# Kernel optimization log

Hardware: AMD Instinct MI355X
Metric: run time of the kernel (lower is better)

The kernel has to match this reference:

```python
import jax, jax.numpy as jnp
import numpy as np

WINDOW_SIZE = 11
SIGMA = 1.5
DATA_RANGE = 1.0
C1 = (0.01 * DATA_RANGE) ** 2
C2 = (0.03 * DATA_RANGE) ** 2


def _gaussian_window(size: int, sigma: float) -> jnp.ndarray:
    coords = jnp.arange(size, dtype=jnp.float32) - size // 2
    g = jnp.exp(-(coords ** 2) / (2.0 * sigma ** 2))
    g = g / g.sum()
    w2d = g[:, None] * g[None, :]
    return w2d[None, None, :, :]  # (O=1, I=1, K, K)


def _conv_same(x, window):
    pad = WINDOW_SIZE // 2
    return jax.lax.conv_general_dilated(
        x, window,
        window_strides=(1, 1),
        padding=((pad, pad), (pad, pad)),
        dimension_numbers=("NCHW", "OIHW", "NCHW"),
    )


def setup_inputs() -> dict:
    key = jax.random.key(0)
    kx, ky = jax.random.split(key)
    B, C, H, W = 64, 1, 512, 512
    x = jax.random.uniform(kx, (B, C, H, W), dtype=jnp.float32)
    y = jax.random.uniform(ky, (B, C, H, W), dtype=jnp.float32)
    return {"x": x, "y": y}


def reference(x, y):
    window = _gaussian_window(WINDOW_SIZE, SIGMA)
    mu_x = _conv_same(x, window)
    mu_y = _conv_same(y, window)
    mu_x_sq = mu_x * mu_x
    mu_y_sq = mu_y * mu_y
    mu_xy = mu_x * mu_y
    sigma_x_sq = _conv_same(x * x, window) - mu_x_sq
    sigma_y_sq = _conv_same(y * y, window) - mu_y_sq
    sigma_xy = _conv_same(x * y, window) - mu_xy
    num = (2.0 * mu_xy + C1) * (2.0 * sigma_xy + C2)
    den = (mu_x_sq + mu_y_sq + C1) * (sigma_x_sq + sigma_y_sq + C2)
    ssim_map = num / den
    ssim_val = ssim_map.mean(axis=(1, 2, 3))  # (B,)
    loss = 1.0 - ssim_val
    return loss.mean()  # reduction='mean'
```

## Files before the change

kernel.cpp:

```cpp
#include <hip/hip_runtime.h>
#include <hip/hip_fp16.h>

typedef _Float16 f16x8 __attribute__((ext_vector_type(8)));
typedef _Float16 f16x2 __attribute__((ext_vector_type(2)));
typedef float    f32x4 __attribute__((ext_vector_type(4)));
typedef float    f32x2 __attribute__((ext_vector_type(2)));

#define IMG    512
#define NIMG   64
#define TS_C   64
#define NBLK   (NIMG * 8 * 8)
#define UNITS  1680
#define PLANE  (42 * 80)
#define HTS    36

#define C1F    1.0e-4f
#define C2F    9.0e-4f
#define INVSUM 0.26601174f

__device__ __forceinline__ uint2 cvt4h(f32x4 a) {
    __half2 p0 = __floats2half2_rn(a[0], a[1]);
    __half2 p1 = __floats2half2_rn(a[2], a[3]);
    uint2 r; r.x = *reinterpret_cast<uint*>(&p0); r.y = *reinterpret_cast<uint*>(&p1);
    return r;
}

__device__ __forceinline__ f16x2 pkrtz(float a, float b) {
    auto t = __builtin_amdgcn_cvt_pkrtz(a, b);
    return __builtin_bit_cast(f16x2, t);
}

__global__ __launch_bounds__(256, 3)
void ssim_main(const float* __restrict__ x, const float* __restrict__ y,
               float* __restrict__ partial) {
    __shared__ __align__(16) float  XYpF[UNITS * 4];
    __shared__ __align__(16) __half Ht[5][TS_C][HTS];
    __shared__ _Float16 wtab[64];
    __shared__ float red[4];

    const int tid  = threadIdx.x;
    const int lane = tid & 63;
    const int wv   = tid >> 6;
    const int l16  = lane & 15;
    const int g16  = lane >> 4;
    const int n0   = wv * 16;

    const int img = blockIdx.z;
    const int by  = blockIdx.y;
    const int c0  = blockIdx.x * TS_C;
    const float* xb = x + (size_t)img * IMG * IMG;
    const float* yb = y + (size_t)img * IMG * IMG;

    const bool interior = (blockIdx.x >= 1) & (blockIdx.x <= 6) & (by >= 1) & (by <= 6);

    if (tid < 64) {
        int d = tid - 18;
        float t = (float)(d - 5);
        float v = __expf(-t * t * (1.0f / 4.5f)) * INVSUM;
        wtab[tid] = ((unsigned)d <= 10u) ? (_Float16)v : (_Float16)0.0f;
    }

    const int row0 = tid / 20;
    const int c00  = tid - row0 * 20;

    auto zfill = [&]() {
        #pragma unroll
        for (int i = 0; i < 7; ++i)
            if (i < 6 || tid < UNITS - 6 * 256)
                *(f32x4*)&XYpF[(i * 256 + tid) * 4] = (f32x4){0.f, 0.f, 0.f, 0.f};
    };

    auto stage = [&](int r0t) {
        int row_u = row0, slot = c00, rm = row0;
        #pragma unroll
        for (int i = 0; i < 7; ++i) {
            int c4 = slot - rm; if (c4 < 0) c4 += 20;
            bool ya = row_u >= 42;
            int  rp = ya ? row_u - 42 : row_u;
            int  gr = r0t - 5 + rp;
            int  gc = c0 - 8 + c4 * 4;
            const float* src = (ya ? yb : xb) + (size_t)gr * IMG + gc;
            float* dst = &XYpF[(i * 256 + wv * 64) * 4];
            bool tailok = (i < 6) | (tid < UNITS - 6 * 256);
            bool ok = interior ? tailok
                    : (tailok & ((unsigned)gr < (unsigned)IMG)
                              & ((unsigned)gc <= (unsigned)(IMG - 4)));
            if (ok)
                __builtin_amdgcn_global_load_lds(
                    (const __attribute__((address_space(1))) void*)src,
                    (__attribute__((address_space(3))) void*)dst, 16, 0, 0);
            slot += 16; row_u += 12; rm += 12;
            if (slot >= 20) { slot -= 20; row_u += 1; rm += 1; }
            if (rm >= 20) rm -= 20;
        }
    };

    const int hcol = n0 + l16;
    f32x2 ssum2 = {0.0f, 0.0f};
    f16x8 WhB, WvA;

    union UH { f16x8 v; f16x2 p[4]; };

    auto hpass = [&](int g, int sb) {
        int srow = g * 16 + l16;
        if (srow > 41) srow = 41;
        const int cu0 = wv * 4 + g16 * 2;
        int sx0 = srow * 20 + (cu0 + srow) % 20;
        int sx1 = srow * 20 + (cu0 + 1 + srow) % 20;
        int ry  = srow + 42;
        int sy0 = ry * 20 + (cu0 + ry) % 20;
        int sy1 = ry * 20 + (cu0 + 1 + ry) % 20;
        f32x4 xlo = *(const f32x4*)&XYpF[sx0 * 4];
        f32x4 xhi = *(const f32x4*)&XYpF[sx1 * 4];
        f32x4 ylo = *(const f32x4*)&XYpF[sy0 * 4];
        f32x4 yhi = *(const f32x4*)&XYpF[sy1 * 4];
        UH ux, uy;
        ux.p[0] = pkrtz(xlo[0], xlo[1]); ux.p[1] = pkrtz(xlo[2], xlo[3]);
        ux.p[2] = pkrtz(xhi[0], xhi[1]); ux.p[3] = pkrtz(xhi[2], xhi[3]);
        uy.p[0] = pkrtz(ylo[0], ylo[1]); uy.p[1] = pkrtz(ylo[2], ylo[3]);
        uy.p[2] = pkrtz(yhi[0], yhi[1]); uy.p[3] = pkrtz(yhi[2], yhi[3]);
        f16x8 xf = ux.v, yf = uy.v;
        f16x8 xx = xf * xf;
        f16x8 yy = yf * yf;
        f16x8 xy = xf * yf;
        f32x4 z = {0.f, 0.f, 0.f, 0.f};
        f32x4 aX  = __builtin_amdgcn_mfma_f32_16x16x32_f16(xf, WhB, z, 0, 0, 0);
        f32x4 aY  = __builtin_amdgcn_mfma_f32_16x16x32_f16(yf, WhB, z, 0, 0, 0);
        f32x4 aXX = __builtin_amdgcn_mfma_f32_16x16x32_f16(xx, WhB, z, 0, 0, 0);
        f32x4 aYY = __builtin_amdgcn_mfma_f32_16x16x32_f16(yy, WhB, z, 0, 0, 0);
        f32x4 aXY = __builtin_amdgcn_mfma_f32_16x16x32_f16(xy, WhB, z, 0, 0, 0);
        int hrow = sb + g16 * 4;
        *(uint2*)&Ht[0][hcol][hrow] = cvt4h(aX);
        *(uint2*)&Ht[1][hcol][hrow] = cvt4h(aY);
        *(uint2*)&Ht[2][hcol][hrow] = cvt4h(aXX);
        *(uint2*)&Ht[3][hcol][hrow] = cvt4h(aYY);
        *(uint2*)&Ht[4][hcol][hrow] = cvt4h(aXY);
    };

    auto vpass = [&](int mt) {
        int ko = (mt * 16 + g16 * 8) & 31;
        f16x8 b0 = *(const f16x8*)&Ht[0][hcol][ko];
        f16x8 b1 = *(const f16x8*)&Ht[1][hcol][ko];
        f16x8 b2 = *(const f16x8*)&Ht[2][hcol][ko];
        f16x8 b3 = *(const f16x8*)&Ht[3][hcol][ko];
        f16x8 b4 = *(const f16x8*)&Ht[4][hcol][ko];
        f32x4 z = {0.f, 0.f, 0.f, 0.f};
        f32x4 cX  = __builtin_amdgcn_mfma_f32_16x16x32_f16(WvA, b0, z, 0, 0, 0);
        f32x4 cY  = __builtin_amdgcn_mfma_f32_16x16x32_f16(WvA, b1, z, 0, 0, 0);
        f32x4 cXX = __builtin_amdgcn_mfma_f32_16x16x32_f16(WvA, b2, z, 0, 0, 0);
        f32x4 cYY = __builtin_amdgcn_mfma_f32_16x16x32_f16(WvA, b3, z, 0, 0, 0);
        f32x4 cXY = __builtin_amdgcn_mfma_f32_16x16x32_f16(WvA, b4, z, 0, 0, 0);
        #pragma unroll
        for (int h = 0; h < 2; ++h) {
            f32x2 mx  = {cX [2*h], cX [2*h+1]};
            f32x2 my  = {cY [2*h], cY [2*h+1]};
            f32x2 exx = {cXX[2*h], cXX[2*h+1]};
            f32x2 eyy = {cYY[2*h], cYY[2*h+1]};
            f32x2 exy = {cXY[2*h], cXY[2*h+1]};
            f32x2 mxx = mx * mx, myy = my * my, mxy = mx * my;
            f32x2 vx  = exx - mxx;
            f32x2 vy  = eyy - myy;
            f32x2 vxy = exy - mxy;
            f32x2 num = (2.0f * mxy + C1F) * (2.0f * vxy + C2F);
            f32x2 den = (mxx + myy + C1F) * (vx + vy + C2F);
            f32x2 r;
            r[0] = __builtin_amdgcn_rcpf(den[0]);
            r[1] = __builtin_amdgcn_rcpf(den[1]);
            ssum2 += num * r;
        }
    };

    auto compute = [&]() {
        hpass(0, 0); hpass(1, 16); vpass(0); hpass(2, 0); vpass(1);
    };

    const int r0a = by * 64;
    const int r0b = by * 64 + 32;

    if (!interior) { zfill(); __syncthreads(); }
    stage(r0a);
    __syncthreads();

    {
        const int idx0 = g16 * 8 - l16 + 15;
        _Float16 bv[11];
        #pragma unroll
        for (int j = 0; j < 11; ++j) bv[j] = wtab[idx0 + j];
        #pragma unroll
        for (int j = 0; j < 8; ++j) WhB[j] = bv[j];
        #pragma unroll
        for (int j = 0; j < 8; ++j) WvA[j] = bv[j + 3];
    }

    compute();
    __syncthreads();
    if (!interior) { zfill(); __syncthreads(); }
    stage(r0b);
    __syncthreads();
    compute();

    float ssum = ssum2[0] + ssum2[1];
    #pragma unroll
    for (int off = 32; off > 0; off >>= 1)
        ssum += __shfl_down(ssum, off, 64);
    if ((tid & 63) == 0) red[tid >> 6] = ssum;
    __syncthreads();
    if (tid == 0) {
        float tot = red[0] + red[1] + red[2] + red[3];
        int bi = (img * gridDim.y + by) * gridDim.x + blockIdx.x;
        partial[bi] = tot;
    }
}

__global__ __launch_bounds__(1024)
void ssim_final(const float* __restrict__ partial, float* __restrict__ out) {
    __shared__ float red[16];
    float s = 0.0f;
    for (int i = threadIdx.x; i < NBLK; i += 1024) s += partial[i];
    #pragma unroll
    for (int off = 32; off > 0; off >>= 1)
        s += __shfl_down(s, off, 64);
    if ((threadIdx.x & 63) == 0) red[threadIdx.x >> 6] = s;
    __syncthreads();
    if (threadIdx.x == 0) {
        float tot = 0.0f;
        #pragma unroll
        for (int i = 0; i < 16; ++i) tot += red[i];
        out[0] = 1.0f - tot * (1.0f / 16777216.0f);
    }
}

extern "C" void kernel_launch(void* const* d_in, const int* in_sizes, int n_in,
                              void* d_out, int out_size, void* d_ws, size_t ws_size,
                              hipStream_t stream) {
    const float* x = (const float*)d_in[0];
    const float* y = (const float*)d_in[1];
    float* out     = (float*)d_out;
    float* partial = (float*)d_ws;

    dim3 grid(IMG / TS_C, 8, NIMG);
    ssim_main<<<grid, 256, 0, stream>>>(x, y, partial);
    ssim_final<<<1, 1024, 0, stream>>>(partial, out);
}
```

Before: 49.72 us.

## Pipeline LDS staging with fp16 conversion buffer and four row tiles per block

Each block now processes four 32-row tiles instead of two, halving the grid in y. Staged fp32 data is first converted into a separate fp16 LDS buffer in natural layout. This lets the next tile's async global-to-LDS load overlap the MFMA compute of the current tile, and it simplifies the hpass reads to straight f16x8 loads. It costs more LDS, so occupancy drops to 2 blocks per CU, and it adds an extra conversion pass and LDS round trip per tile.

```diff
diff --git a/kernel.cpp b/kernel.cpp
--- a/kernel.cpp
+++ b/kernel.cpp
@@ -9,9 +9,10 @@
 #define IMG    512
 #define NIMG   64
 #define TS_C   64
-#define NBLK   (NIMG * 8 * 8)
+#define TILES  4
+#define NBLK   (NIMG * 4 * 8)
 #define UNITS  1680
-#define PLANE  (42 * 80)
+#define XST    80
 #define HTS    36
 
 #define C1F    1.0e-4f
@@ -25,15 +26,11 @@
     return r;
 }
 
-__device__ __forceinline__ f16x2 pkrtz(float a, float b) {
-    auto t = __builtin_amdgcn_cvt_pkrtz(a, b);
-    return __builtin_bit_cast(f16x2, t);
-}
-
-__global__ __launch_bounds__(256, 3)
+__global__ __launch_bounds__(256, 2)
 void ssim_main(const float* __restrict__ x, const float* __restrict__ y,
                float* __restrict__ partial) {
-    __shared__ __align__(16) float  XYpF[UNITS * 4];
+    __shared__ __align__(16) float  F[UNITS * 4];
+    __shared__ __align__(16) __half H16[2 * 42 * XST];
     __shared__ __align__(16) __half Ht[5][TS_C][HTS];
     __shared__ _Float16 wtab[64];
     __shared__ float red[4];
@@ -51,7 +48,7 @@
     const float* xb = x + (size_t)img * IMG * IMG;
     const float* yb = y + (size_t)img * IMG * IMG;
 
-    const bool interior = (blockIdx.x >= 1) & (blockIdx.x <= 6) & (by >= 1) & (by <= 6);
+    const bool interior = (blockIdx.x >= 1) & (blockIdx.x <= 6) & (by >= 1) & (by <= 2);
 
     if (tid < 64) {
         int d = tid - 18;
@@ -67,20 +64,20 @@
         #pragma unroll
         for (int i = 0; i < 7; ++i)
             if (i < 6 || tid < UNITS - 6 * 256)
-                *(f32x4*)&XYpF[(i * 256 + tid) * 4] = (f32x4){0.f, 0.f, 0.f, 0.f};
+                *(f32x4*)&F[(i * 256 + tid) * 4] = (f32x4){0.f, 0.f, 0.f, 0.f};
+        __asm__ volatile("s_waitcnt lgkmcnt(0)");
     };
 
     auto stage = [&](int r0t) {
-        int row_u = row0, slot = c00, rm = row0;
+        int row_u = row0, c4 = c00;
         #pragma unroll
         for (int i = 0; i < 7; ++i) {
-            int c4 = slot - rm; if (c4 < 0) c4 += 20;
             bool ya = row_u >= 42;
             int  rp = ya ? row_u - 42 : row_u;
             int  gr = r0t - 5 + rp;
             int  gc = c0 - 8 + c4 * 4;
             const float* src = (ya ? yb : xb) + (size_t)gr * IMG + gc;
-            float* dst = &XYpF[(i * 256 + wv * 64) * 4];
+            float* dst = &F[(i * 256 + wv * 64) * 4];
             bool tailok = (i < 6) | (tid < UNITS - 6 * 256);
             bool ok = interior ? tailok
                     : (tailok & ((unsigned)gr < (unsigned)IMG)
@@ -89,9 +86,24 @@
                 __builtin_amdgcn_global_load_lds(
                     (const __attribute__((address_space(1))) void*)src,
                     (__attribute__((address_space(3))) void*)dst, 16, 0, 0);
-            slot += 16; row_u += 12; rm += 12;
-            if (slot >= 20) { slot -= 20; row_u += 1; rm += 1; }
-            if (rm >= 20) rm -= 20;
+            c4 += 16; row_u += 12;
+            if (c4 >= 20) { c4 -= 20; row_u += 1; }
+        }
+    };
+
+    auto convert = [&]() {
+        int row_u = row0, c4 = c00;
+        #pragma unroll
+        for (int i = 0; i < 7; ++i) {
+            if (i < 6 || tid < UNITS - 6 * 256) {
+                f32x4 v = *(const f32x4*)&F[(i * 256 + tid) * 4];
+                __half2 p0 = __floats2half2_rn(v[0], v[1]);
+                __half2 p1 = __floats2half2_rn(v[2], v[3]);
+                uint2 w; w.x = *(uint*)&p0; w.y = *(uint*)&p1;
+                *(uint2*)&H16[row_u * XST + c4 * 4] = w;
+            }
+            c4 += 16; row_u += 12;
+            if (c4 >= 20) { c4 -= 20; row_u += 1; }
         }
     };
 
@@ -99,27 +111,12 @@
     f32x2 ssum2 = {0.0f, 0.0f};
     f16x8 WhB, WvA;
 
-    union UH { f16x8 v; f16x2 p[4]; };
-
     auto hpass = [&](int g, int sb) {
         int srow = g * 16 + l16;
         if (srow > 41) srow = 41;
-        const int cu0 = wv * 4 + g16 * 2;
-        int sx0 = srow * 20 + (cu0 + srow) % 20;
-        int sx1 = srow * 20 + (cu0 + 1 + srow) % 20;
-        int ry  = srow + 42;
-        int sy0 = ry * 20 + (cu0 + ry) % 20;
-        int sy1 = ry * 20 + (cu0 + 1 + ry) % 20;
-        f32x4 xlo = *(const f32x4*)&XYpF[sx0 * 4];
-        f32x4 xhi = *(const f32x4*)&XYpF[sx1 * 4];
-        f32x4 ylo = *(const f32x4*)&XYpF[sy0 * 4];
-        f32x4 yhi = *(const f32x4*)&XYpF[sy1 * 4];
-        UH ux, uy;
-        ux.p[0] = pkrtz(xlo[0], xlo[1]); ux.p[1] = pkrtz(xlo[2], xlo[3]);
-        ux.p[2] = pkrtz(xhi[0], xhi[1]); ux.p[3] = pkrtz(xhi[2], xhi[3]);
-        uy.p[0] = pkrtz(ylo[0], ylo[1]); uy.p[1] = pkrtz(ylo[2], ylo[3]);
-        uy.p[2] = pkrtz(yhi[0], yhi[1]); uy.p[3] = pkrtz(yhi[2], yhi[3]);
-        f16x8 xf = ux.v, yf = uy.v;
+        int off = srow * XST + n0 + g16 * 8;
+        f16x8 xf = *(const f16x8*)&H16[off];
+        f16x8 yf = *(const f16x8*)&H16[42 * XST + off];
         f16x8 xx = xf * xf;
         f16x8 yy = yf * yf;
         f16x8 xy = xf * yf;
@@ -174,11 +171,10 @@
         hpass(0, 0); hpass(1, 16); vpass(0); hpass(2, 0); vpass(1);
     };
 
-    const int r0a = by * 64;
-    const int r0b = by * 64 + 32;
-
-    if (!interior) { zfill(); __syncthreads(); }
-    stage(r0a);
+    const int rbase = by * (TILES * 32);
+
+    if (!interior) zfill();
+    stage(rbase);
     __syncthreads();
 
     {
@@ -192,12 +188,17 @@
         for (int j = 0; j < 8; ++j) WvA[j] = bv[j + 3];
     }
 
-    compute();
-    __syncthreads();
-    if (!interior) { zfill(); __syncthreads(); }
-    stage(r0b);
-    __syncthreads();
-    compute();
+    #pragma unroll
+    for (int k = 0; k < TILES; ++k) {
+        convert();
+        __syncthreads();
+        if (k + 1 < TILES) {
+            if (!interior) zfill();
+            stage(rbase + (k + 1) * 32);
+        }
+        compute();
+        __syncthreads();
+    }
 
     float ssum = ssum2[0] + ssum2[1];
     #pragma unroll
@@ -238,7 +239,7 @@
     float* out     = (float*)d_out;
     float* partial = (float*)d_ws;
 
-    dim3 grid(IMG / TS_C, 8, NIMG);
+    dim3 grid(IMG / TS_C, 4, NIMG);
     ssim_main<<<grid, 256, 0, stream>>>(x, y, partial);
     ssim_final<<<1, 1024, 0, stream>>>(partial, out);
 }
```

Measured after the change: 54.67 us. +10.0%, slower.
